# Kernel tuning notes

Hardware: AMD Instinct MI355X
Metric: run time of the kernel (lower is better)

## Reference

```python
import jax, jax.numpy as jnp
import numpy as np

B, T, I, H, O = 8192, 180, 7, 64, 16

def setup_inputs() -> dict:
    key = jax.random.key(0)
    ks = jax.random.split(key, 8)
    s_ih = 1.0 / np.sqrt(H)
    x = jax.random.normal(ks[0], (B, T, I), dtype=jnp.float32)
    # PyTorch nn.LSTM param layout: [4H, in] with gate order i, f, g, o
    W_ih = jax.random.uniform(ks[1], (4 * H, I), jnp.float32, -s_ih, s_ih)
    W_hh = jax.random.uniform(ks[2], (4 * H, H), jnp.float32, -s_ih, s_ih)
    b_ih = jax.random.uniform(ks[3], (4 * H,), jnp.float32, -s_ih, s_ih)
    b_hh = jax.random.uniform(ks[4], (4 * H,), jnp.float32, -s_ih, s_ih)
    W_fc = jax.random.uniform(ks[5], (O, H), jnp.float32, -s_ih, s_ih)
    b_fc = jax.random.uniform(ks[6], (O,), jnp.float32, -s_ih, s_ih)
    return {"x": x, "W_ih": W_ih, "W_hh": W_hh, "b_ih": b_ih,
            "b_hh": b_hh, "W_fc": W_fc, "b_fc": b_fc}

def reference(x, W_ih, W_hh, b_ih, b_hh, W_fc, b_fc):
    x = x.reshape(-1, T, I)
    b = b_ih + b_hh
    # precompute input projections for all timesteps: [T, B, 4H]
    xg = jnp.einsum('bti,gi->tbg', x, W_ih) + b

    def step(carry, xg_t):
        h, c = carry
        gates = xg_t + h @ W_hh.T  # [B, 4H]
        i_g, f_g, g_g, o_g = jnp.split(gates, 4, axis=-1)
        i_g = jax.nn.sigmoid(i_g)
        f_g = jax.nn.sigmoid(f_g)
        g_g = jnp.tanh(g_g)
        o_g = jax.nn.sigmoid(o_g)
        c = f_g * c + i_g * g_g
        h = o_g * jnp.tanh(c)
        return (h, c), None

    h0 = jnp.zeros((x.shape[0], H), dtype=x.dtype)
    c0 = jnp.zeros((x.shape[0], H), dtype=x.dtype)
    (h_last, _), _ = jax.lax.scan(step, (h0, c0), xg)
    return h_last @ W_fc.T + b_fc  # [B, O]
```

## Files before the change

kernel.cpp:

```cpp
#include <hip/hip_runtime.h>
#include <math.h>

#ifndef __has_builtin
#define __has_builtin(x) 0
#endif

#if __has_builtin(__builtin_amdgcn_rcpf)
#define FAST_RCP(x) __builtin_amdgcn_rcpf(x)
#else
#define FAST_RCP(x) (1.0f / (x))
#endif

#if __has_builtin(__builtin_amdgcn_exp2f)
#define FAST_EXP2(x) __builtin_amdgcn_exp2f(x)
#else
#define FAST_EXP2(x) exp2f(x)
#endif

typedef _Float16 half8 __attribute__((ext_vector_type(8)));
typedef _Float16 half2v __attribute__((ext_vector_type(2)));
typedef float f32x4 __attribute__((ext_vector_type(4)));
typedef float f32x2 __attribute__((ext_vector_type(2)));

constexpr int T_STEPS = 180;
constexpr int I_DIM   = 7;
constexpr int HDIM    = 64;
constexpr int BT      = 16;
constexpr int NCH     = 12;
constexpr int CH_HALF = BT * 8;
constexpr int XSTR    = 136;

__global__ __launch_bounds__(512, 4) void lstm_mfma_kernel(
    const float* __restrict__ x,
    const float* __restrict__ W_ih,
    const float* __restrict__ W_hh,
    const float* __restrict__ b_ih,
    const float* __restrict__ b_hh,
    const float* __restrict__ W_fc,
    const float* __restrict__ b_fc,
    float* __restrict__ out) {
    __shared__ alignas(16) _Float16 Bbuf[2][NCH][BT][8];
    __shared__ alignas(16) _Float16 xstage[T_STEPS * XSTR];
    __shared__ alignas(16) float hlds[BT][HDIM + 4];

    const int tid  = (int)threadIdx.x;
    const int w    = tid >> 6;
    const int lane = tid & 63;
    const int q    = lane >> 4;
    const int n15  = lane & 15;
    const long bbase = (long)blockIdx.x * BT;

    half8 afrag[2][3];
#pragma unroll
    for (int pt = 0; pt < 2; ++pt) {
        const int gate = 2 * pt + ((n15 >> 1) & 1);
        const int unit = 8 * w + 2 * (n15 >> 2) + (n15 & 1);
        const int grow = gate * HDIM + unit;
        const float scl = (gate == 2) ? 2.88539008177792681472f
                                      : -1.44269504088896340736f;
#pragma unroll
        for (int kc = 0; kc < 3; ++kc) {
#pragma unroll
            for (int j = 0; j < 8; ++j) {
                const int k = kc * 32 + q * 8 + j;
                float v;
                if (k < I_DIM)            v = W_ih[grow * I_DIM + k];
                else if (k == I_DIM)      v = b_ih[grow] + b_hh[grow];
                else if (k < 8 + HDIM)    v = W_hh[grow * HDIM + (k - 8)];
                else                      v = 0.0f;
                afrag[pt][kc][j] = (_Float16)(scl * v);
            }
        }
    }

    for (int idx = tid; idx < BT * T_STEPS * I_DIM; idx += 512) {
        const int n = idx / (T_STEPS * I_DIM);
        const int r = idx - n * (T_STEPS * I_DIM);
        const int t = r / I_DIM, i = r - t * I_DIM;
        xstage[t * XSTR + n * 8 + i] =
            (_Float16)x[(bbase + n) * (T_STEPS * I_DIM) + r];
    }
    for (int idx = tid; idx < T_STEPS * BT; idx += 512)
        xstage[(idx >> 4) * XSTR + (idx & 15) * 8 + 7] = (_Float16)1.0f;
    for (int idx = tid; idx < 2 * NCH * CH_HALF; idx += 512)
        ((_Float16*)Bbuf)[idx] = (_Float16)0.0f;
    __syncthreads();

    const int u0 = 8 * w + 2 * q;

    const _Float16* const rb0 = &Bbuf[0][q][n15][0];
    const _Float16* const rb1 = &Bbuf[1][q][n15][0];
    const _Float16* xb0 = (q == 0) ? &xstage[0 * XSTR + n15 * 8] : rb0;
    const _Float16* xb1 = (q == 0) ? &xstage[1 * XSTR + n15 * 8] : rb1;
    const int xadv = (q == 0) ? 2 * XSTR : 0;
    half2v* const hw0 = (half2v*)&Bbuf[0][1 + w][n15][2 * q];
    half2v* const hw1 = (half2v*)&Bbuf[1][1 + w][n15][2 * q];

    f32x2 cp = {0.0f, 0.0f};
    f32x2 hp = {0.0f, 0.0f};
    const f32x4 zq = {0.0f, 0.0f, 0.0f, 0.0f};

#define LSTM_CELL2(A0, A1)                                                     \
    {                                                                          \
        f32x2 Ap, Fp, Ep, Op, Rp, Cp, rD;                                      \
        Ap[0] = FAST_EXP2(A0[0]); Ap[1] = FAST_EXP2(A0[1]);                    \
        Fp[0] = FAST_EXP2(A0[2]); Fp[1] = FAST_EXP2(A0[3]);                    \
        Ep[0] = FAST_EXP2(A1[0]); Ep[1] = FAST_EXP2(A1[1]);                    \
        const f32x2 Pp = (Ap + 1.0f) * (Ep + 1.0f);                            \
        const f32x2 Qp = Fp + 1.0f;                                            \
        const f32x2 PQ = Pp * Qp;                                              \
        Rp[0] = FAST_RCP(PQ[0]); Rp[1] = FAST_RCP(PQ[1]);                      \
        cp = (cp * Pp + (Ep - 1.0f) * Qp) * Rp;                                \
        Op[0] = FAST_EXP2(A1[2]); Op[1] = FAST_EXP2(A1[3]);                    \
        f32x2 cs = cp * 2.88539008177792681472f;                               \
        cs[0] = fminf(fmaxf(cs[0], -80.0f), 80.0f);                            \
        cs[1] = fminf(fmaxf(cs[1], -80.0f), 80.0f);                            \
        Cp[0] = FAST_EXP2(cs[0]); Cp[1] = FAST_EXP2(cs[1]);                    \
        const f32x2 Dp = (Op + 1.0f) * (Cp + 1.0f);                            \
        rD[0] = FAST_RCP(Dp[0]); rD[1] = FAST_RCP(Dp[1]);                      \
        hp = (Cp - 1.0f) * rD;                                                 \
    }

#define LSTM_STEP(RB, XB, HW)                                                  \
    {                                                                          \
        const half8 bf0 = *(const half8*)(XB);                                 \
        const half8 bf1 = *(const half8*)((RB) + 4 * CH_HALF);                 \
        const half8 bf2 = *(const half8*)((RB) + 8 * CH_HALF);                 \
        f32x4 acc0 = __builtin_amdgcn_mfma_f32_16x16x32_f16(afrag[0][0], bf0, zq, 0, 0, 0); \
        f32x4 acc1 = __builtin_amdgcn_mfma_f32_16x16x32_f16(afrag[1][0], bf0, zq, 0, 0, 0); \
        acc0 = __builtin_amdgcn_mfma_f32_16x16x32_f16(afrag[0][1], bf1, acc0, 0, 0, 0); \
        acc1 = __builtin_amdgcn_mfma_f32_16x16x32_f16(afrag[1][1], bf1, acc1, 0, 0, 0); \
        acc0 = __builtin_amdgcn_mfma_f32_16x16x32_f16(afrag[0][2], bf2, acc0, 0, 0, 0); \
        acc1 = __builtin_amdgcn_mfma_f32_16x16x32_f16(afrag[1][2], bf2, acc1, 0, 0, 0); \
        LSTM_CELL2(acc0, acc1)                                                 \
        *(HW) = (half2v){(_Float16)hp[0], (_Float16)hp[1]};                    \
        __syncthreads();                                                       \
    }

    for (int t = 0; t < T_STEPS; t += 2) {
        LSTM_STEP(rb0, xb0, hw1)
        LSTM_STEP(rb1, xb1, hw0)
        xb0 += xadv;
        xb1 += xadv;
    }
#undef LSTM_STEP
#undef LSTM_CELL2

    *(f32x2*)&hlds[n15][u0] = hp;
    __syncthreads();
    if (tid < 256) {
        const int b = tid >> 4, j = tid & 15;
        float s = b_fc[j];
#pragma unroll 8
        for (int u = 0; u < HDIM; ++u)
            s += hlds[b][u] * W_fc[j * HDIM + u];
        out[(bbase + b) * 16 + j] = s;
    }
}

extern "C" void kernel_launch(void* const* d_in, const int* in_sizes, int n_in,
                              void* d_out, int out_size, void* d_ws, size_t ws_size,
                              hipStream_t stream) {
    const float* x    = (const float*)d_in[0];
    const float* W_ih = (const float*)d_in[1];
    const float* W_hh = (const float*)d_in[2];
    const float* b_ih = (const float*)d_in[3];
    const float* b_hh = (const float*)d_in[4];
    const float* W_fc = (const float*)d_in[5];
    const float* b_fc = (const float*)d_in[6];
    float* out = (float*)d_out;

    const int B = in_sizes[0] / (T_STEPS * I_DIM);
    const int grid = B / BT;

    lstm_mfma_kernel<<<grid, 512, 0, stream>>>(x, W_ih, W_hh, b_ih, b_hh,
                                               W_fc, b_fc, out);
}
```

Baseline: 191.7 us.

## Interleave two batch groups per block and stage x in time chunks

Each block now processes two independent 16-sample batch groups. Their MFMA chains and cell updates are interleaved so each barrier covers two independent recurrences, which gives the scheduler more independent work to hide MFMA and transcendental latency. The x input is staged into shared memory in three 60-step chunks instead of all 180 steps, keeping LDS use bounded despite the doubled per-block state. The cost is half as many blocks, a lower launch-bounds occupancy hint (2 instead of 4), higher register pressure, and extra restaging syncs between chunks.

```diff
diff --git a/kernel.cpp b/kernel.cpp
--- a/kernel.cpp
+++ b/kernel.cpp
@@ -26,11 +26,13 @@
 constexpr int I_DIM   = 7;
 constexpr int HDIM    = 64;
 constexpr int BT      = 16;
+constexpr int NGRP    = 2;
+constexpr int TCH     = 60;
 constexpr int NCH     = 12;
 constexpr int CH_HALF = BT * 8;
 constexpr int XSTR    = 136;
 
-__global__ __launch_bounds__(512, 4) void lstm_mfma_kernel(
+__global__ __launch_bounds__(512, 2) void lstm_mfma_kernel(
     const float* __restrict__ x,
     const float* __restrict__ W_ih,
     const float* __restrict__ W_hh,
@@ -39,16 +41,16 @@
     const float* __restrict__ W_fc,
     const float* __restrict__ b_fc,
     float* __restrict__ out) {
-    __shared__ alignas(16) _Float16 Bbuf[2][NCH][BT][8];
-    __shared__ alignas(16) _Float16 xstage[T_STEPS * XSTR];
-    __shared__ alignas(16) float hlds[BT][HDIM + 4];
+    __shared__ alignas(16) _Float16 Bbuf[NGRP][2][NCH][BT][8];
+    __shared__ alignas(16) _Float16 xstage[NGRP][TCH * XSTR];
+    __shared__ alignas(16) float hlds[NGRP][BT][HDIM + 4];
 
     const int tid  = (int)threadIdx.x;
     const int w    = tid >> 6;
     const int lane = tid & 63;
     const int q    = lane >> 4;
     const int n15  = lane & 15;
-    const long bbase = (long)blockIdx.x * BT;
+    const long bbase = (long)blockIdx.x * (NGRP * BT);
 
     half8 afrag[2][3];
 #pragma unroll
@@ -73,34 +75,43 @@
         }
     }
 
-    for (int idx = tid; idx < BT * T_STEPS * I_DIM; idx += 512) {
-        const int n = idx / (T_STEPS * I_DIM);
-        const int r = idx - n * (T_STEPS * I_DIM);
-        const int t = r / I_DIM, i = r - t * I_DIM;
-        xstage[t * XSTR + n * 8 + i] =
-            (_Float16)x[(bbase + n) * (T_STEPS * I_DIM) + r];
-    }
-    for (int idx = tid; idx < T_STEPS * BT; idx += 512)
-        xstage[(idx >> 4) * XSTR + (idx & 15) * 8 + 7] = (_Float16)1.0f;
-    for (int idx = tid; idx < 2 * NCH * CH_HALF; idx += 512)
+#define STAGE_X(TC)                                                            \
+    for (int idx = tid; idx < NGRP * BT * TCH * 8; idx += 512) {               \
+        const int i = idx & 7;                                                 \
+        const int n = (idx >> 3) & 15;                                         \
+        const int t = (idx >> 7) % TCH;                                        \
+        const int g = (idx >> 7) / TCH;                                        \
+        float v = 1.0f;                                                        \
+        if (i < I_DIM)                                                         \
+            v = x[(bbase + g * BT + n) * (T_STEPS * I_DIM) +                   \
+                  ((TC) * TCH + t) * I_DIM + i];                               \
+        xstage[g][t * XSTR + n * 8 + i] = (_Float16)v;                         \
+    }
+
+    STAGE_X(0)
+    for (int idx = tid; idx < NGRP * 2 * NCH * CH_HALF; idx += 512)
         ((_Float16*)Bbuf)[idx] = (_Float16)0.0f;
     __syncthreads();
 
     const int u0 = 8 * w + 2 * q;
 
-    const _Float16* const rb0 = &Bbuf[0][q][n15][0];
-    const _Float16* const rb1 = &Bbuf[1][q][n15][0];
-    const _Float16* xb0 = (q == 0) ? &xstage[0 * XSTR + n15 * 8] : rb0;
-    const _Float16* xb1 = (q == 0) ? &xstage[1 * XSTR + n15 * 8] : rb1;
+    const _Float16* const rbA0 = &Bbuf[0][0][q][n15][0];
+    const _Float16* const rbA1 = &Bbuf[0][1][q][n15][0];
+    const _Float16* const rbB0 = &Bbuf[1][0][q][n15][0];
+    const _Float16* const rbB1 = &Bbuf[1][1][q][n15][0];
+    half2v* const hwA0 = (half2v*)&Bbuf[0][0][1 + w][n15][2 * q];
+    half2v* const hwA1 = (half2v*)&Bbuf[0][1][1 + w][n15][2 * q];
+    half2v* const hwB0 = (half2v*)&Bbuf[1][0][1 + w][n15][2 * q];
+    half2v* const hwB1 = (half2v*)&Bbuf[1][1][1 + w][n15][2 * q];
+    const _Float16* const xsA = &xstage[0][n15 * 8];
+    const _Float16* const xsB = &xstage[1][n15 * 8];
     const int xadv = (q == 0) ? 2 * XSTR : 0;
-    half2v* const hw0 = (half2v*)&Bbuf[0][1 + w][n15][2 * q];
-    half2v* const hw1 = (half2v*)&Bbuf[1][1 + w][n15][2 * q];
-
-    f32x2 cp = {0.0f, 0.0f};
-    f32x2 hp = {0.0f, 0.0f};
+
+    f32x2 cpA = {0.0f, 0.0f}, hpA = {0.0f, 0.0f};
+    f32x2 cpB = {0.0f, 0.0f}, hpB = {0.0f, 0.0f};
     const f32x4 zq = {0.0f, 0.0f, 0.0f, 0.0f};
 
-#define LSTM_CELL2(A0, A1)                                                     \
+#define LSTM_CELL2(A0, A1, CP, HP)                                             \
     {                                                                          \
         f32x2 Ap, Fp, Ep, Op, Rp, Cp, rD;                                      \
         Ap[0] = FAST_EXP2(A0[0]); Ap[1] = FAST_EXP2(A0[1]);                    \
@@ -110,51 +121,73 @@
         const f32x2 Qp = Fp + 1.0f;                                            \
         const f32x2 PQ = Pp * Qp;                                              \
         Rp[0] = FAST_RCP(PQ[0]); Rp[1] = FAST_RCP(PQ[1]);                      \
-        cp = (cp * Pp + (Ep - 1.0f) * Qp) * Rp;                                \
+        CP = (CP * Pp + (Ep - 1.0f) * Qp) * Rp;                                \
         Op[0] = FAST_EXP2(A1[2]); Op[1] = FAST_EXP2(A1[3]);                    \
-        f32x2 cs = cp * 2.88539008177792681472f;                               \
+        f32x2 cs = CP * 2.88539008177792681472f;                               \
         cs[0] = fminf(fmaxf(cs[0], -80.0f), 80.0f);                            \
         cs[1] = fminf(fmaxf(cs[1], -80.0f), 80.0f);                            \
         Cp[0] = FAST_EXP2(cs[0]); Cp[1] = FAST_EXP2(cs[1]);                    \
         const f32x2 Dp = (Op + 1.0f) * (Cp + 1.0f);                            \
         rD[0] = FAST_RCP(Dp[0]); rD[1] = FAST_RCP(Dp[1]);                      \
-        hp = (Cp - 1.0f) * rD;                                                 \
-    }
-
-#define LSTM_STEP(RB, XB, HW)                                                  \
+        HP = (Cp - 1.0f) * rD;                                                 \
+    }
+
+#define LSTM_STEP2(XBA, RBA, HWA, XBB, RBB, HWB)                               \
     {                                                                          \
-        const half8 bf0 = *(const half8*)(XB);                                 \
-        const half8 bf1 = *(const half8*)((RB) + 4 * CH_HALF);                 \
-        const half8 bf2 = *(const half8*)((RB) + 8 * CH_HALF);                 \
-        f32x4 acc0 = __builtin_amdgcn_mfma_f32_16x16x32_f16(afrag[0][0], bf0, zq, 0, 0, 0); \
-        f32x4 acc1 = __builtin_amdgcn_mfma_f32_16x16x32_f16(afrag[1][0], bf0, zq, 0, 0, 0); \
-        acc0 = __builtin_amdgcn_mfma_f32_16x16x32_f16(afrag[0][1], bf1, acc0, 0, 0, 0); \
-        acc1 = __builtin_amdgcn_mfma_f32_16x16x32_f16(afrag[1][1], bf1, acc1, 0, 0, 0); \
-        acc0 = __builtin_amdgcn_mfma_f32_16x16x32_f16(afrag[0][2], bf2, acc0, 0, 0, 0); \
-        acc1 = __builtin_amdgcn_mfma_f32_16x16x32_f16(afrag[1][2], bf2, acc1, 0, 0, 0); \
-        LSTM_CELL2(acc0, acc1)                                                 \
-        *(HW) = (half2v){(_Float16)hp[0], (_Float16)hp[1]};                    \
+        const half8 bA0 = *(const half8*)(XBA);                                \
+        const half8 bA1 = *(const half8*)((RBA) + 4 * CH_HALF);                \
+        const half8 bA2 = *(const half8*)((RBA) + 8 * CH_HALF);                \
+        const half8 bB0 = *(const half8*)(XBB);                                \
+        const half8 bB1 = *(const half8*)((RBB) + 4 * CH_HALF);                \
+        const half8 bB2 = *(const half8*)((RBB) + 8 * CH_HALF);                \
+        f32x4 aA0 = __builtin_amdgcn_mfma_f32_16x16x32_f16(afrag[0][0], bA0, zq, 0, 0, 0); \
+        f32x4 aB0 = __builtin_amdgcn_mfma_f32_16x16x32_f16(afrag[0][0], bB0, zq, 0, 0, 0); \
+        f32x4 aA1 = __builtin_amdgcn_mfma_f32_16x16x32_f16(afrag[1][0], bA0, zq, 0, 0, 0); \
+        f32x4 aB1 = __builtin_amdgcn_mfma_f32_16x16x32_f16(afrag[1][0], bB0, zq, 0, 0, 0); \
+        aA0 = __builtin_amdgcn_mfma_f32_16x16x32_f16(afrag[0][1], bA1, aA0, 0, 0, 0); \
+        aB0 = __builtin_amdgcn_mfma_f32_16x16x32_f16(afrag[0][1], bB1, aB0, 0, 0, 0); \
+        aA1 = __builtin_amdgcn_mfma_f32_16x16x32_f16(afrag[1][1], bA1, aA1, 0, 0, 0); \
+        aB1 = __builtin_amdgcn_mfma_f32_16x16x32_f16(afrag[1][1], bB1, aB1, 0, 0, 0); \
+        aA0 = __builtin_amdgcn_mfma_f32_16x16x32_f16(afrag[0][2], bA2, aA0, 0, 0, 0); \
+        aB0 = __builtin_amdgcn_mfma_f32_16x16x32_f16(afrag[0][2], bB2, aB0, 0, 0, 0); \
+        aA1 = __builtin_amdgcn_mfma_f32_16x16x32_f16(afrag[1][2], bA2, aA1, 0, 0, 0); \
+        aB1 = __builtin_amdgcn_mfma_f32_16x16x32_f16(afrag[1][2], bB2, aB1, 0, 0, 0); \
+        LSTM_CELL2(aA0, aA1, cpA, hpA)                                         \
+        LSTM_CELL2(aB0, aB1, cpB, hpB)                                         \
+        *(HWA) = (half2v){(_Float16)hpA[0], (_Float16)hpA[1]};                 \
+        *(HWB) = (half2v){(_Float16)hpB[0], (_Float16)hpB[1]};                 \
         __syncthreads();                                                       \
     }
 
-    for (int t = 0; t < T_STEPS; t += 2) {
-        LSTM_STEP(rb0, xb0, hw1)
-        LSTM_STEP(rb1, xb1, hw0)
-        xb0 += xadv;
-        xb1 += xadv;
-    }
-#undef LSTM_STEP
+    for (int tc = 0; tc < T_STEPS / TCH; ++tc) {
+        if (tc) {
+            STAGE_X(tc)
+            __syncthreads();
+        }
+        const _Float16* xbA0 = (q == 0) ? xsA : rbA0;
+        const _Float16* xbA1 = (q == 0) ? xsA + XSTR : rbA1;
+        const _Float16* xbB0 = (q == 0) ? xsB : rbB0;
+        const _Float16* xbB1 = (q == 0) ? xsB + XSTR : rbB1;
+        for (int tt = 0; tt < TCH; tt += 2) {
+            LSTM_STEP2(xbA0, rbA0, hwA1, xbB0, rbB0, hwB1)
+            LSTM_STEP2(xbA1, rbA1, hwA0, xbB1, rbB1, hwB0)
+            xbA0 += xadv; xbA1 += xadv; xbB0 += xadv; xbB1 += xadv;
+        }
+    }
+#undef LSTM_STEP2
 #undef LSTM_CELL2
-
-    *(f32x2*)&hlds[n15][u0] = hp;
+#undef STAGE_X
+
+    *(f32x2*)&hlds[0][n15][u0] = hpA;
+    *(f32x2*)&hlds[1][n15][u0] = hpB;
     __syncthreads();
-    if (tid < 256) {
-        const int b = tid >> 4, j = tid & 15;
+    {
+        const int g = tid >> 8, b = (tid >> 4) & 15, j = tid & 15;
         float s = b_fc[j];
 #pragma unroll 8
         for (int u = 0; u < HDIM; ++u)
-            s += hlds[b][u] * W_fc[j * HDIM + u];
-        out[(bbase + b) * 16 + j] = s;
+            s += hlds[g][b][u] * W_fc[j * HDIM + u];
+        out[(bbase + g * BT + b) * 16 + j] = s;
     }
 }
 
@@ -171,7 +204,7 @@
     float* out = (float*)d_out;
 
     const int B = in_sizes[0] / (T_STEPS * I_DIM);
-    const int grid = B / BT;
+    const int grid = B / (NGRP * BT);
 
     lstm_mfma_kernel<<<grid, 512, 0, stream>>>(x, W_ih, W_hh, b_ih, b_hh,
                                                W_fc, b_fc, out);
```

New measurement: 226.1 us. +17.9%, slower.

## Halve waves per block with two hidden tiles per wave and chunked x staging

Applied to the files above, without the earlier changes.

Each block now runs 256 threads (4 waves) instead of 512, and each wave computes two 8-unit hidden tiles per step using four MFMA accumulator chains. The input sequence is staged into LDS in two 90-step chunks rather than all 180 steps, shrinking shared memory so more blocks can fit per CU. This cuts barrier cost and adds independent MFMA work per wave. In exchange, each wave's serial cell math per timestep roughly doubles, and a mid-sequence restaging pass is added.

```diff
diff --git a/kernel.cpp b/kernel.cpp
--- a/kernel.cpp
+++ b/kernel.cpp
@@ -26,11 +26,12 @@
 constexpr int I_DIM   = 7;
 constexpr int HDIM    = 64;
 constexpr int BT      = 16;
+constexpr int TCH     = 90;
 constexpr int NCH     = 12;
 constexpr int CH_HALF = BT * 8;
 constexpr int XSTR    = 136;
 
-__global__ __launch_bounds__(512, 4) void lstm_mfma_kernel(
+__global__ __launch_bounds__(256, 4) void lstm_mfma_kernel(
     const float* __restrict__ x,
     const float* __restrict__ W_ih,
     const float* __restrict__ W_hh,
@@ -40,7 +41,7 @@
     const float* __restrict__ b_fc,
     float* __restrict__ out) {
     __shared__ alignas(16) _Float16 Bbuf[2][NCH][BT][8];
-    __shared__ alignas(16) _Float16 xstage[T_STEPS * XSTR];
+    __shared__ alignas(16) _Float16 xstage[TCH * XSTR];
     __shared__ alignas(16) float hlds[BT][HDIM + 4];
 
     const int tid  = (int)threadIdx.x;
@@ -50,11 +51,11 @@
     const int n15  = lane & 15;
     const long bbase = (long)blockIdx.x * BT;
 
-    half8 afrag[2][3];
+    half8 afrag[4][3];
 #pragma unroll
-    for (int pt = 0; pt < 2; ++pt) {
-        const int gate = 2 * pt + ((n15 >> 1) & 1);
-        const int unit = 8 * w + 2 * (n15 >> 2) + (n15 & 1);
+    for (int pt = 0; pt < 4; ++pt) {
+        const int gate = 2 * (pt & 1) + ((n15 >> 1) & 1);
+        const int unit = 16 * w + 8 * (pt >> 1) + 2 * (n15 >> 2) + (n15 & 1);
         const int grow = gate * HDIM + unit;
         const float scl = (gate == 2) ? 2.88539008177792681472f
                                       : -1.44269504088896340736f;
@@ -73,34 +74,37 @@
         }
     }
 
-    for (int idx = tid; idx < BT * T_STEPS * I_DIM; idx += 512) {
-        const int n = idx / (T_STEPS * I_DIM);
-        const int r = idx - n * (T_STEPS * I_DIM);
-        const int t = r / I_DIM, i = r - t * I_DIM;
-        xstage[t * XSTR + n * 8 + i] =
-            (_Float16)x[(bbase + n) * (T_STEPS * I_DIM) + r];
-    }
-    for (int idx = tid; idx < T_STEPS * BT; idx += 512)
-        xstage[(idx >> 4) * XSTR + (idx & 15) * 8 + 7] = (_Float16)1.0f;
-    for (int idx = tid; idx < 2 * NCH * CH_HALF; idx += 512)
+#define STAGE_X(TC)                                                            \
+    for (int idx = tid; idx < BT * TCH * 8; idx += 256) {                      \
+        const int i = idx & 7;                                                 \
+        const int n = (idx >> 3) & 15;                                         \
+        const int t = idx >> 7;                                                \
+        float v = 1.0f;                                                        \
+        if (i < I_DIM)                                                         \
+            v = x[(bbase + n) * (T_STEPS * I_DIM) +                            \
+                  ((TC) * TCH + t) * I_DIM + i];                               \
+        xstage[t * XSTR + n * 8 + i] = (_Float16)v;                            \
+    }
+
+    STAGE_X(0)
+    for (int idx = tid; idx < 2 * NCH * CH_HALF; idx += 256)
         ((_Float16*)Bbuf)[idx] = (_Float16)0.0f;
     __syncthreads();
 
-    const int u0 = 8 * w + 2 * q;
-
     const _Float16* const rb0 = &Bbuf[0][q][n15][0];
     const _Float16* const rb1 = &Bbuf[1][q][n15][0];
-    const _Float16* xb0 = (q == 0) ? &xstage[0 * XSTR + n15 * 8] : rb0;
-    const _Float16* xb1 = (q == 0) ? &xstage[1 * XSTR + n15 * 8] : rb1;
+    half2v* const hwA0 = (half2v*)&Bbuf[0][1 + 2 * w + 0][n15][2 * q];
+    half2v* const hwA1 = (half2v*)&Bbuf[1][1 + 2 * w + 0][n15][2 * q];
+    half2v* const hwB0 = (half2v*)&Bbuf[0][1 + 2 * w + 1][n15][2 * q];
+    half2v* const hwB1 = (half2v*)&Bbuf[1][1 + 2 * w + 1][n15][2 * q];
+    const _Float16* const xs = &xstage[n15 * 8];
     const int xadv = (q == 0) ? 2 * XSTR : 0;
-    half2v* const hw0 = (half2v*)&Bbuf[0][1 + w][n15][2 * q];
-    half2v* const hw1 = (half2v*)&Bbuf[1][1 + w][n15][2 * q];
-
-    f32x2 cp = {0.0f, 0.0f};
-    f32x2 hp = {0.0f, 0.0f};
+
+    f32x2 cp0 = {0.0f, 0.0f}, hp0 = {0.0f, 0.0f};
+    f32x2 cp1 = {0.0f, 0.0f}, hp1 = {0.0f, 0.0f};
     const f32x4 zq = {0.0f, 0.0f, 0.0f, 0.0f};
 
-#define LSTM_CELL2(A0, A1)                                                     \
+#define LSTM_CELL2(A0, A1, CP, HP)                                             \
     {                                                                          \
         f32x2 Ap, Fp, Ep, Op, Rp, Cp, rD;                                      \
         Ap[0] = FAST_EXP2(A0[0]); Ap[1] = FAST_EXP2(A0[1]);                    \
@@ -110,45 +114,63 @@
         const f32x2 Qp = Fp + 1.0f;                                            \
         const f32x2 PQ = Pp * Qp;                                              \
         Rp[0] = FAST_RCP(PQ[0]); Rp[1] = FAST_RCP(PQ[1]);                      \
-        cp = (cp * Pp + (Ep - 1.0f) * Qp) * Rp;                                \
+        CP = (CP * Pp + (Ep - 1.0f) * Qp) * Rp;                                \
         Op[0] = FAST_EXP2(A1[2]); Op[1] = FAST_EXP2(A1[3]);                    \
-        f32x2 cs = cp * 2.88539008177792681472f;                               \
+        f32x2 cs = CP * 2.88539008177792681472f;                               \
         cs[0] = fminf(fmaxf(cs[0], -80.0f), 80.0f);                            \
         cs[1] = fminf(fmaxf(cs[1], -80.0f), 80.0f);                            \
         Cp[0] = FAST_EXP2(cs[0]); Cp[1] = FAST_EXP2(cs[1]);                    \
         const f32x2 Dp = (Op + 1.0f) * (Cp + 1.0f);                            \
         rD[0] = FAST_RCP(Dp[0]); rD[1] = FAST_RCP(Dp[1]);                      \
-        hp = (Cp - 1.0f) * rD;                                                 \
-    }
-
-#define LSTM_STEP(RB, XB, HW)                                                  \
+        HP = (Cp - 1.0f) * rD;                                                 \
+    }
+
+#define LSTM_STEP(RB, XB, HWA, HWB)                                            \
     {                                                                          \
         const half8 bf0 = *(const half8*)(XB);                                 \
         const half8 bf1 = *(const half8*)((RB) + 4 * CH_HALF);                 \
         const half8 bf2 = *(const half8*)((RB) + 8 * CH_HALF);                 \
-        f32x4 acc0 = __builtin_amdgcn_mfma_f32_16x16x32_f16(afrag[0][0], bf0, zq, 0, 0, 0); \
-        f32x4 acc1 = __builtin_amdgcn_mfma_f32_16x16x32_f16(afrag[1][0], bf0, zq, 0, 0, 0); \
-        acc0 = __builtin_amdgcn_mfma_f32_16x16x32_f16(afrag[0][1], bf1, acc0, 0, 0, 0); \
-        acc1 = __builtin_amdgcn_mfma_f32_16x16x32_f16(afrag[1][1], bf1, acc1, 0, 0, 0); \
-        acc0 = __builtin_amdgcn_mfma_f32_16x16x32_f16(afrag[0][2], bf2, acc0, 0, 0, 0); \
-        acc1 = __builtin_amdgcn_mfma_f32_16x16x32_f16(afrag[1][2], bf2, acc1, 0, 0, 0); \
-        LSTM_CELL2(acc0, acc1)                                                 \
-        *(HW) = (half2v){(_Float16)hp[0], (_Float16)hp[1]};                    \
+        f32x4 a00 = __builtin_amdgcn_mfma_f32_16x16x32_f16(afrag[0][0], bf0, zq, 0, 0, 0); \
+        f32x4 a01 = __builtin_amdgcn_mfma_f32_16x16x32_f16(afrag[1][0], bf0, zq, 0, 0, 0); \
+        f32x4 a10 = __builtin_amdgcn_mfma_f32_16x16x32_f16(afrag[2][0], bf0, zq, 0, 0, 0); \
+        f32x4 a11 = __builtin_amdgcn_mfma_f32_16x16x32_f16(afrag[3][0], bf0, zq, 0, 0, 0); \
+        a00 = __builtin_amdgcn_mfma_f32_16x16x32_f16(afrag[0][1], bf1, a00, 0, 0, 0); \
+        a01 = __builtin_amdgcn_mfma_f32_16x16x32_f16(afrag[1][1], bf1, a01, 0, 0, 0); \
+        a10 = __builtin_amdgcn_mfma_f32_16x16x32_f16(afrag[2][1], bf1, a10, 0, 0, 0); \
+        a11 = __builtin_amdgcn_mfma_f32_16x16x32_f16(afrag[3][1], bf1, a11, 0, 0, 0); \
+        a00 = __builtin_amdgcn_mfma_f32_16x16x32_f16(afrag[0][2], bf2, a00, 0, 0, 0); \
+        a01 = __builtin_amdgcn_mfma_f32_16x16x32_f16(afrag[1][2], bf2, a01, 0, 0, 0); \
+        a10 = __builtin_amdgcn_mfma_f32_16x16x32_f16(afrag[2][2], bf2, a10, 0, 0, 0); \
+        a11 = __builtin_amdgcn_mfma_f32_16x16x32_f16(afrag[3][2], bf2, a11, 0, 0, 0); \
+        LSTM_CELL2(a00, a01, cp0, hp0)                                         \
+        LSTM_CELL2(a10, a11, cp1, hp1)                                         \
+        *(HWA) = (half2v){(_Float16)hp0[0], (_Float16)hp0[1]};                 \
+        *(HWB) = (half2v){(_Float16)hp1[0], (_Float16)hp1[1]};                 \
         __syncthreads();                                                       \
     }
 
-    for (int t = 0; t < T_STEPS; t += 2) {
-        LSTM_STEP(rb0, xb0, hw1)
-        LSTM_STEP(rb1, xb1, hw0)
-        xb0 += xadv;
-        xb1 += xadv;
+    for (int tc = 0; tc < T_STEPS / TCH; ++tc) {
+        if (tc) {
+            STAGE_X(tc)
+            __syncthreads();
+        }
+        const _Float16* xb0 = (q == 0) ? xs : rb0;
+        const _Float16* xb1 = (q == 0) ? xs + XSTR : rb1;
+        for (int tt = 0; tt < TCH; tt += 2) {
+            LSTM_STEP(rb0, xb0, hwA1, hwB1)
+            LSTM_STEP(rb1, xb1, hwA0, hwB0)
+            xb0 += xadv;
+            xb1 += xadv;
+        }
     }
 #undef LSTM_STEP
 #undef LSTM_CELL2
-
-    *(f32x2*)&hlds[n15][u0] = hp;
+#undef STAGE_X
+
+    *(f32x2*)&hlds[n15][16 * w + 2 * q]     = hp0;
+    *(f32x2*)&hlds[n15][16 * w + 8 + 2 * q] = hp1;
     __syncthreads();
-    if (tid < 256) {
+    {
         const int b = tid >> 4, j = tid & 15;
         float s = b_fc[j];
 #pragma unroll 8
@@ -173,6 +195,6 @@
     const int B = in_sizes[0] / (T_STEPS * I_DIM);
     const int grid = B / BT;
 
-    lstm_mfma_kernel<<<grid, 512, 0, stream>>>(x, W_ih, W_hh, b_ih, b_hh,
+    lstm_mfma_kernel<<<grid, 256, 0, stream>>>(x, W_ih, W_hh, b_ih, b_hh,
                                                W_fc, b_fc, out);
 }
```

After: 212.3 us. +10.7%, slower.

## Hoist input-projection MFMA off the recurrent critical path and shrink h buffer

Applied to the files above, without the earlier changes.

Splits the K dimension so the x/bias chunk is handled by a dedicated MFMA pair computed one step ahead (nacc) and overlapped with the cell nonlinearity, leaving only two dependent MFMAs on h per step. The h buffer drops from 12 to 8 chunks, and a padded zero timestep is added to xstage so the lookahead read stays in bounds. It also adds s_setprio around the step and a sched_barrier before the block sync to favour the recurrent wave. The cost is two extra accumulator registers and a slightly larger LDS footprint for x.

```diff
diff --git a/kernel.cpp b/kernel.cpp
--- a/kernel.cpp
+++ b/kernel.cpp
@@ -26,7 +26,6 @@
 constexpr int I_DIM   = 7;
 constexpr int HDIM    = 64;
 constexpr int BT      = 16;
-constexpr int NCH     = 12;
 constexpr int CH_HALF = BT * 8;
 constexpr int XSTR    = 136;
 
@@ -39,8 +38,8 @@
     const float* __restrict__ W_fc,
     const float* __restrict__ b_fc,
     float* __restrict__ out) {
-    __shared__ alignas(16) _Float16 Bbuf[2][NCH][BT][8];
-    __shared__ alignas(16) _Float16 xstage[T_STEPS * XSTR];
+    __shared__ alignas(16) _Float16 Bbuf[2][8][BT][8];
+    __shared__ alignas(16) _Float16 xstage[(T_STEPS + 1) * XSTR];
     __shared__ alignas(16) float hlds[BT][HDIM + 4];
 
     const int tid  = (int)threadIdx.x;
@@ -62,27 +61,31 @@
         for (int kc = 0; kc < 3; ++kc) {
 #pragma unroll
             for (int j = 0; j < 8; ++j) {
-                const int k = kc * 32 + q * 8 + j;
                 float v;
-                if (k < I_DIM)            v = W_ih[grow * I_DIM + k];
-                else if (k == I_DIM)      v = b_ih[grow] + b_hh[grow];
-                else if (k < 8 + HDIM)    v = W_hh[grow * HDIM + (k - 8)];
-                else                      v = 0.0f;
+                if (kc == 0) {
+                    if (q != 0)          v = 0.0f;
+                    else if (j < I_DIM)  v = W_ih[grow * I_DIM + j];
+                    else                 v = b_ih[grow] + b_hh[grow];
+                } else {
+                    v = W_hh[grow * HDIM + (kc - 1) * 32 + 8 * q + j];
+                }
                 afrag[pt][kc][j] = (_Float16)(scl * v);
             }
         }
     }
 
-    for (int idx = tid; idx < BT * T_STEPS * I_DIM; idx += 512) {
-        const int n = idx / (T_STEPS * I_DIM);
-        const int r = idx - n * (T_STEPS * I_DIM);
-        const int t = r / I_DIM, i = r - t * I_DIM;
-        xstage[t * XSTR + n * 8 + i] =
-            (_Float16)x[(bbase + n) * (T_STEPS * I_DIM) + r];
+    for (int idx = tid; idx < BT * (T_STEPS + 1) * 8; idx += 512) {
+        const int i = idx & 7;
+        const int n = (idx >> 3) & 15;
+        const int t = idx >> 7;
+        float v = 1.0f;
+        if (i < I_DIM)
+            v = (t < T_STEPS)
+                    ? x[(bbase + n) * (T_STEPS * I_DIM) + t * I_DIM + i]
+                    : 0.0f;
+        xstage[t * XSTR + n * 8 + i] = (_Float16)v;
     }
-    for (int idx = tid; idx < T_STEPS * BT; idx += 512)
-        xstage[(idx >> 4) * XSTR + (idx & 15) * 8 + 7] = (_Float16)1.0f;
-    for (int idx = tid; idx < 2 * NCH * CH_HALF; idx += 512)
+    for (int idx = tid; idx < 2 * 8 * CH_HALF; idx += 512)
         ((_Float16*)Bbuf)[idx] = (_Float16)0.0f;
     __syncthreads();
 
@@ -90,11 +93,9 @@
 
     const _Float16* const rb0 = &Bbuf[0][q][n15][0];
     const _Float16* const rb1 = &Bbuf[1][q][n15][0];
-    const _Float16* xb0 = (q == 0) ? &xstage[0 * XSTR + n15 * 8] : rb0;
-    const _Float16* xb1 = (q == 0) ? &xstage[1 * XSTR + n15 * 8] : rb1;
-    const int xadv = (q == 0) ? 2 * XSTR : 0;
-    half2v* const hw0 = (half2v*)&Bbuf[0][1 + w][n15][2 * q];
-    half2v* const hw1 = (half2v*)&Bbuf[1][1 + w][n15][2 * q];
+    half2v* const hw0 = (half2v*)&Bbuf[0][w][n15][2 * q];
+    half2v* const hw1 = (half2v*)&Bbuf[1][w][n15][2 * q];
+    const _Float16* xb = &xstage[XSTR + n15 * 8];
 
     f32x2 cp = {0.0f, 0.0f};
     f32x2 hp = {0.0f, 0.0f};
@@ -121,27 +122,36 @@
         hp = (Cp - 1.0f) * rD;                                                 \
     }
 
-#define LSTM_STEP(RB, XB, HW)                                                  \
+    f32x4 nacc0, nacc1;
+    {
+        const half8 bfx0 = *(const half8*)&xstage[0 * XSTR + n15 * 8];
+        nacc0 = __builtin_amdgcn_mfma_f32_16x16x32_f16(afrag[0][0], bfx0, zq, 0, 0, 0);
+        nacc1 = __builtin_amdgcn_mfma_f32_16x16x32_f16(afrag[1][0], bfx0, zq, 0, 0, 0);
+    }
+
+#define LSTM_STEP(RB, HW, XO)                                                  \
     {                                                                          \
-        const half8 bf0 = *(const half8*)(XB);                                 \
-        const half8 bf1 = *(const half8*)((RB) + 4 * CH_HALF);                 \
-        const half8 bf2 = *(const half8*)((RB) + 8 * CH_HALF);                 \
-        f32x4 acc0 = __builtin_amdgcn_mfma_f32_16x16x32_f16(afrag[0][0], bf0, zq, 0, 0, 0); \
-        f32x4 acc1 = __builtin_amdgcn_mfma_f32_16x16x32_f16(afrag[1][0], bf0, zq, 0, 0, 0); \
-        acc0 = __builtin_amdgcn_mfma_f32_16x16x32_f16(afrag[0][1], bf1, acc0, 0, 0, 0); \
-        acc1 = __builtin_amdgcn_mfma_f32_16x16x32_f16(afrag[1][1], bf1, acc1, 0, 0, 0); \
+        __builtin_amdgcn_s_setprio(1);                                         \
+        const half8 bf1 = *(const half8*)(RB);                                 \
+        const half8 bf2 = *(const half8*)((RB) + 4 * CH_HALF);                 \
+        f32x4 acc0 = __builtin_amdgcn_mfma_f32_16x16x32_f16(afrag[0][1], bf1, nacc0, 0, 0, 0); \
+        f32x4 acc1 = __builtin_amdgcn_mfma_f32_16x16x32_f16(afrag[1][1], bf1, nacc1, 0, 0, 0); \
         acc0 = __builtin_amdgcn_mfma_f32_16x16x32_f16(afrag[0][2], bf2, acc0, 0, 0, 0); \
         acc1 = __builtin_amdgcn_mfma_f32_16x16x32_f16(afrag[1][2], bf2, acc1, 0, 0, 0); \
+        const half8 bfx = *(const half8*)(xb + (XO));                          \
+        nacc0 = __builtin_amdgcn_mfma_f32_16x16x32_f16(afrag[0][0], bfx, zq, 0, 0, 0); \
+        nacc1 = __builtin_amdgcn_mfma_f32_16x16x32_f16(afrag[1][0], bfx, zq, 0, 0, 0); \
         LSTM_CELL2(acc0, acc1)                                                 \
         *(HW) = (half2v){(_Float16)hp[0], (_Float16)hp[1]};                    \
+        __builtin_amdgcn_s_setprio(0);                                         \
+        __builtin_amdgcn_sched_barrier(0);                                     \
         __syncthreads();                                                       \
     }
 
     for (int t = 0; t < T_STEPS; t += 2) {
-        LSTM_STEP(rb0, xb0, hw1)
-        LSTM_STEP(rb1, xb1, hw0)
-        xb0 += xadv;
-        xb1 += xadv;
+        LSTM_STEP(rb0, hw1, 0)
+        LSTM_STEP(rb1, hw0, XSTR)
+        xb += 2 * XSTR;
     }
 #undef LSTM_STEP
 #undef LSTM_CELL2
```

Result: no change. 194.7 us (+1.6%).
